# Optimization experiments

Hardware: AMD Instinct MI355X
Metric: run time of the kernel (lower is better)

The kernel has to match this reference:

```python
import jax, jax.numpy as jnp
import numpy as np

NUM_STEPS = 2001   # int(Tsim/dt) + 1 = int(0.002/1e-6) + 1
LEAK = 0.95
THRESHOLD = 0.3


def setup_inputs() -> dict:
    key = jax.random.key(0)
    x = jax.random.normal(key, (16, 2048), dtype=jnp.float32)
    return {"x": x}


def reference(x):
    # Leaky-integrate-and-fire scan with hard reset.
    # NOTE: the original forward computes PoissonGen(input) each step but never
    # uses the result, so it is omitted (no effect on the math).
    def step(v, _):
        v = LEAK * v + (1.0 - LEAK) * x          # leak + drive
        spk = v > THRESHOLD                        # fire
        v = jnp.where(spk, 0.0, v)                 # hard reset (stored in v_t)
        return v, (v, spk.astype(jnp.int32))

    v0 = jnp.zeros_like(x)
    v_last, (v_t, s_t) = jax.lax.scan(step, v0, None, length=NUM_STEPS)
    s_last = s_t[-1]
    # matches torch return: (spikes, v, v_t, s_t) with histories stacked [T, B, N]
    return s_last, v_last, v_t, s_t
```

## Files before the change

kernel.cpp:

```cpp
#include <hip/hip_runtime.h>


#define T_STEPS 2001

__global__ __launch_bounds__(128) void lif_scan_kernel(
    const float* __restrict__ x,
    float* __restrict__ s_last,
    float* __restrict__ v_last,
    float* __restrict__ v_t,
    float* __restrict__ s_t,
    int n)
{
    const int i = blockIdx.x * blockDim.x + threadIdx.x;
    if (i >= n) return;

    const float LEAK   = 0.95f;
    const float DRIVE  = 0.05f;
    const float THRESH = 0.3f;

    const float xv    = x[i];
    const float drive = __fmul_rn(DRIVE, xv);

    float v    = 0.0f;
    float spkf = 0.0f;
    size_t off = (size_t)i;

    #pragma unroll 4
    for (int t = 0; t < T_STEPS; ++t) {
        v = __fadd_rn(__fmul_rn(LEAK, v), drive);
        const bool spk = v > THRESH;
        v    = spk ? 0.0f : v;
        spkf = spk ? 1.0f : 0.0f;
        v_t[off] = v;
        s_t[off] = spkf;
        off += (size_t)n;
    }

    s_last[i] = spkf;
    v_last[i] = v;
}

extern "C" void kernel_launch(void* const* d_in, const int* in_sizes, int n_in,
                              void* d_out, int out_size, void* d_ws, size_t ws_size,
                              hipStream_t stream)
{
    const float* x = (const float*)d_in[0];
    const int n = in_sizes[0];

    float* out    = (float*)d_out;
    float* s_last = out;
    float* v_last = out + n;
    float* v_t    = out + 2 * (size_t)n;
    float* s_t    = out + 2 * (size_t)n + (size_t)T_STEPS * (size_t)n;

    const int block = 128;
    const int grid  = (n + block - 1) / block;
    lif_scan_kernel<<<grid, block, 0, stream>>>(x, s_last, v_last, v_t, s_t, n);
}
```

Measured before the change: 82.05 us.

## Split time scan into chunks with recompute, vectorize float4, nontemporal stores

The time axis is split into 16 chunks, each handled by its own block. Each block recomputes the recurrence from t=0 up to its chunk start without storing anything, then writes only its chunk. Each thread now handles four neurons through float4 vector loads and stores, and history writes use nontemporal stores. The aim is to expose far more parallelism: the original launched only 256 wavefronts for a 262 MB write-bound kernel. The cost is redundant recompute and hardcoded sizes (32 blocks per chunk, n4 assumed to be 8192).

Result: slower. 96.89 us (+18.1%).

```diff
diff --git a/kernel.cpp b/kernel.cpp
--- a/kernel.cpp
+++ b/kernel.cpp
@@ -1,43 +1,72 @@
 #include <hip/hip_runtime.h>
 
 
+#pragma clang fp contract(off)
+
+typedef float f32x4 __attribute__((ext_vector_type(4)));
+
 #define T_STEPS 2001
+#define NCHUNK  16
+#define CHUNK   126
 
-__global__ __launch_bounds__(128) void lif_scan_kernel(
-    const float* __restrict__ x,
-    float* __restrict__ s_last,
-    float* __restrict__ v_last,
-    float* __restrict__ v_t,
-    float* __restrict__ s_t,
-    int n)
+__global__ __launch_bounds__(256) void lif_chunk_kernel(
+    const f32x4* __restrict__ x4,
+    f32x4*  __restrict__ s_last4,
+    f32x4*  __restrict__ v_last4,
+    f32x4* __restrict__ v_t4,
+    f32x4* __restrict__ s_t4,
+    int n4)
 {
-    const int i = blockIdx.x * blockDim.x + threadIdx.x;
-    if (i >= n) return;
+    #pragma clang fp contract(off)
 
     const float LEAK   = 0.95f;
     const float DRIVE  = 0.05f;
     const float THRESH = 0.3f;
 
-    const float xv    = x[i];
-    const float drive = __fmul_rn(DRIVE, xv);
+    const int bid   = blockIdx.x;
+    const int chunk = bid >> 5;
+    const int nb    = bid & 31;
+    const int tid   = nb * 256 + threadIdx.x;
 
-    float v    = 0.0f;
-    float spkf = 0.0f;
-    size_t off = (size_t)i;
+    const f32x4 xv = x4[tid];
+    f32x4 dr;
+    dr.x = DRIVE * xv.x;
+    dr.y = DRIVE * xv.y;
+    dr.z = DRIVE * xv.z;
+    dr.w = DRIVE * xv.w;
+
+    f32x4 v = (f32x4){0.f, 0.f, 0.f, 0.f};
+
+    const int t0 = chunk * CHUNK;
+    const int t1 = (t0 + CHUNK < T_STEPS) ? (t0 + CHUNK) : T_STEPS;
 
     #pragma unroll 4
-    for (int t = 0; t < T_STEPS; ++t) {
-        v = __fadd_rn(__fmul_rn(LEAK, v), drive);
-        const bool spk = v > THRESH;
-        v    = spk ? 0.0f : v;
-        spkf = spk ? 1.0f : 0.0f;
-        v_t[off] = v;
-        s_t[off] = spkf;
-        off += (size_t)n;
+    for (int t = 0; t < t0; ++t) {
+        v.x = LEAK * v.x + dr.x; v.x = (v.x > THRESH) ? 0.f : v.x;
+        v.y = LEAK * v.y + dr.y; v.y = (v.y > THRESH) ? 0.f : v.y;
+        v.z = LEAK * v.z + dr.z; v.z = (v.z > THRESH) ? 0.f : v.z;
+        v.w = LEAK * v.w + dr.w; v.w = (v.w > THRESH) ? 0.f : v.w;
     }
 
-    s_last[i] = spkf;
-    v_last[i] = v;
+    size_t off = (size_t)t0 * (size_t)n4 + (size_t)tid;
+    f32x4 s = (f32x4){0.f, 0.f, 0.f, 0.f};
+
+    #pragma unroll 2
+    for (int t = t0; t < t1; ++t) {
+        bool k;
+        v.x = LEAK * v.x + dr.x; k = v.x > THRESH; v.x = k ? 0.f : v.x; s.x = k ? 1.f : 0.f;
+        v.y = LEAK * v.y + dr.y; k = v.y > THRESH; v.y = k ? 0.f : v.y; s.y = k ? 1.f : 0.f;
+        v.z = LEAK * v.z + dr.z; k = v.z > THRESH; v.z = k ? 0.f : v.z; s.z = k ? 1.f : 0.f;
+        v.w = LEAK * v.w + dr.w; k = v.w > THRESH; v.w = k ? 0.f : v.w; s.w = k ? 1.f : 0.f;
+        __builtin_nontemporal_store(v, &v_t4[off]);
+        __builtin_nontemporal_store(s, &s_t4[off]);
+        off += (size_t)n4;
+    }
+
+    if (chunk == NCHUNK - 1) {
+        s_last4[tid] = s;
+        v_last4[tid] = v;
+    }
 }
 
 extern "C" void kernel_launch(void* const* d_in, const int* in_sizes, int n_in,
@@ -45,7 +74,8 @@
                               hipStream_t stream)
 {
     const float* x = (const float*)d_in[0];
-    const int n = in_sizes[0];
+    const int n  = in_sizes[0];
+    const int n4 = n / 4;
 
     float* out    = (float*)d_out;
     float* s_last = out;
@@ -53,7 +83,9 @@
     float* v_t    = out + 2 * (size_t)n;
     float* s_t    = out + 2 * (size_t)n + (size_t)T_STEPS * (size_t)n;
 
-    const int block = 128;
-    const int grid  = (n + block - 1) / block;
-    lif_scan_kernel<<<grid, block, 0, stream>>>(x, s_last, v_last, v_t, s_t, n);
+    const int block = 256;
+    const int grid  = (n4 / block) * NCHUNK;
+    lif_chunk_kernel<<<grid, block, 0, stream>>>(
+        (const f32x4*)x, (f32x4*)s_last, (f32x4*)v_last,
+        (f32x4*)v_t, (f32x4*)s_t, n4);
 }
```

## Stage LIF history through LDS to emit 16-byte vectorized global stores

Applied to the files above, without the earlier changes.

Each thread computes 8 time steps into registers, writes them to a double-buffered LDS tile, then the block cooperatively stores the tile as float4 vectors to the v_t and s_t histories. The aim is to cut the number of global store instructions and improve write efficiency for this write-bandwidth-bound scan. It adds a block barrier every 8 steps and assumes n is a multiple of 128, removing the bounds check.

Result: slower. 98.33 us (+19.8%).

```diff
diff --git a/kernel.cpp b/kernel.cpp
--- a/kernel.cpp
+++ b/kernel.cpp
@@ -1,9 +1,15 @@
 #include <hip/hip_runtime.h>
 
 
-#define T_STEPS 2001
+#pragma clang fp contract(off)
 
-__global__ __launch_bounds__(128) void lif_scan_kernel(
+typedef float f32x4 __attribute__((ext_vector_type(4)));
+
+#define T_STEPS  2001
+#define G        8
+#define NGROUPS  250
+
+__global__ __launch_bounds__(128) void lif_lds_kernel(
     const float* __restrict__ x,
     float* __restrict__ s_last,
     float* __restrict__ v_last,
@@ -11,33 +17,65 @@
     float* __restrict__ s_t,
     int n)
 {
-    const int i = blockIdx.x * blockDim.x + threadIdx.x;
-    if (i >= n) return;
+    #pragma clang fp contract(off)
 
-    const float LEAK   = 0.95f;
-    const float DRIVE  = 0.05f;
-    const float THRESH = 0.3f;
+    __shared__ __align__(16) float lds[2][2][G * 128];
 
-    const float xv    = x[i];
-    const float drive = __fmul_rn(DRIVE, xv);
+    const int t   = threadIdx.x;
+    const int bid = blockIdx.x;
+    const int gid = bid * 128 + t;
+    const int n4  = n >> 2;
 
-    float v    = 0.0f;
-    float spkf = 0.0f;
-    size_t off = (size_t)i;
+    f32x4* __restrict__ v_t4 = (f32x4*)v_t;
+    f32x4* __restrict__ s_t4 = (f32x4*)s_t;
 
-    #pragma unroll 4
-    for (int t = 0; t < T_STEPS; ++t) {
-        v = __fadd_rn(__fmul_rn(LEAK, v), drive);
-        const bool spk = v > THRESH;
-        v    = spk ? 0.0f : v;
-        spkf = spk ? 1.0f : 0.0f;
-        v_t[off] = v;
-        s_t[off] = spkf;
-        off += (size_t)n;
+    const float dr = __fmul_rn(0.05f, x[gid]);
+    float v = 0.f;
+
+    for (int tg = 0; tg < NGROUPS; ++tg) {
+        const int db = tg & 1;
+
+        float vb[G], sb[G];
+        #pragma unroll
+        for (int j = 0; j < G; ++j) {
+            float u = __fadd_rn(__fmul_rn(0.95f, v), dr);
+            bool  k = u > 0.3f;
+            v     = k ? 0.f : u;
+            vb[j] = v;
+            sb[j] = k ? 1.f : 0.f;
+        }
+
+        #pragma unroll
+        for (int j = 0; j < G; ++j) {
+            lds[db][0][j * 128 + t] = vb[j];
+            lds[db][1][j * 128 + t] = sb[j];
+        }
+        __syncthreads();
+
+        const int t0 = tg * G;
+        #pragma unroll
+        for (int k = 0; k < 4; ++k) {
+            const int u    = t + k * 128;
+            const int quad = u & 31;
+            const int step = (u >> 5) & (G - 1);
+            const int arr  = u >> 8;
+            const f32x4* lv = (const f32x4*)&lds[db][arr][0];
+            const f32x4  val = lv[step * 32 + quad];
+            f32x4* dst = arr ? s_t4 : v_t4;
+            dst[(size_t)(t0 + step) * n4 + bid * 32 + quad] = val;
+        }
     }
 
-    s_last[i] = spkf;
-    v_last[i] = v;
+    {
+        float u = __fadd_rn(__fmul_rn(0.95f, v), dr);
+        bool  k = u > 0.3f;
+        v = k ? 0.f : u;
+        const float s = k ? 1.f : 0.f;
+        v_t[(size_t)2000 * n + gid] = v;
+        s_t[(size_t)2000 * n + gid] = s;
+        s_last[gid] = s;
+        v_last[gid] = v;
+    }
 }
 
 extern "C" void kernel_launch(void* const* d_in, const int* in_sizes, int n_in,
@@ -54,6 +92,6 @@
     float* s_t    = out + 2 * (size_t)n + (size_t)T_STEPS * (size_t)n;
 
     const int block = 128;
-    const int grid  = (n + block - 1) / block;
-    lif_scan_kernel<<<grid, block, 0, stream>>>(x, s_last, v_last, v_t, s_t, n);
+    const int grid  = n / block;
+    lif_lds_kernel<<<grid, block, 0, stream>>>(x, s_last, v_last, v_t, s_t, n);
 }
```
